# Optimization experiments

Measured on AMD Instinct MI355X. Metric: run time of the kernel, lower is better.

Reference implementation:

```python
import jax, jax.numpy as jnp
import numpy as np

EPS = 1.1920928955078125e-07  # torch fp32 default eps for F.rms_norm
N_HEADS = 16
HEAD_DIM = 128


def apply_rotary_emb(x, cos, sin):
    # x: [B,S,H,D]; cos/sin: [1,S,1,D/2]
    d = x.shape[-1] // 2
    x1, x2 = x[..., :d], x[..., d:]
    return jnp.concatenate([x1 * cos + x2 * sin, -x1 * sin + x2 * cos], axis=-1)


def rms_norm(x):
    # F.rms_norm over last dim, no learned weight
    ms = jnp.mean(jnp.square(x), axis=-1, keepdims=True)
    return x * jax.lax.rsqrt(ms + EPS)


def setup_inputs() -> dict:
    key = jax.random.key(0)
    ks = jax.random.split(key, 7)
    B, S, D = 2, 2048, 2048
    half = HEAD_DIM // 2
    # rotary tables (built like standard RoPE for realism)
    inv_freq = 1.0 / (10000.0 ** (np.arange(0, half, dtype=np.float32) / half))
    t = np.arange(S, dtype=np.float32)
    freqs = np.outer(t, inv_freq)  # [S, D/2]
    cos = jnp.asarray(np.cos(freqs))[None, :, None, :]
    sin = jnp.asarray(np.sin(freqs))[None, :, None, :]
    sd = 1.0 / np.sqrt(D)
    return {
        "x": jax.random.normal(ks[0], (B, S, D), jnp.float32),
        "cos": cos,
        "sin": sin,
        "Wq": jax.random.normal(ks[1], (D, D), jnp.float32) * sd,
        "Wk": jax.random.normal(ks[2], (D, D), jnp.float32) * sd,
        "Wv": jax.random.normal(ks[3], (D, D), jnp.float32) * sd,
        "Wo": jax.random.normal(ks[4], (D, D), jnp.float32) * sd,
    }


def reference(x, cos, sin, Wq, Wk, Wv, Wo):
    B, S, D = x.shape
    H, Hd = N_HEADS, HEAD_DIM
    q = (x @ Wq.T).reshape(B, S, H, Hd)
    k = (x @ Wk.T).reshape(B, S, H, Hd)
    v = (x @ Wv.T).reshape(B, S, H, Hd)
    q = apply_rotary_emb(q, cos[:, :S], sin[:, :S])
    k = apply_rotary_emb(k, cos[:, :S], sin[:, :S])
    q = rms_norm(q) * 1.2  # [B,S,H,Hd]
    k = rms_norm(k) * 1.2
    scale = 1.0 / jnp.sqrt(jnp.asarray(Hd, x.dtype))
    # scores: [B,H,Sq,Sk]
    scores = jnp.einsum("bqhd,bkhd->bhqk", q, k) * scale
    attn = jax.nn.softmax(scores, axis=-1)
    y = jnp.einsum("bhqk,bkhd->bqhd", attn, v).reshape(B, S, D)
    return y @ Wo.T
```

## Files before the change

### kernel.cpp

```cpp
#include <hip/hip_runtime.h>
#include <hip/hip_bf16.h>
#include <math.h>

typedef __bf16 bf16;
typedef __attribute__((ext_vector_type(8))) __bf16 bf16x8;
typedef __attribute__((ext_vector_type(4))) float f32x4;
typedef __attribute__((ext_vector_type(16))) float f32x16;

#define DEV __device__ __forceinline__

DEV void gload16(const void* g, void* l) {
    __builtin_amdgcn_global_load_lds(
        (__attribute__((address_space(1))) void*)(void*)g,
        (__attribute__((address_space(3))) void*)l, 16, 0, 0);
}

DEV unsigned pk2(float a, float b) {
    union { bf16 h[2]; unsigned u; } z;
    z.h[0] = (bf16)a; z.h[1] = (bf16)b;
    return z.u;
}

DEV void plswap(unsigned& a, unsigned& b) {
    asm volatile("v_permlane32_swap_b32 %0, %1" : "+v"(a), "+v"(b));
}

DEV f32x16 mfma32(bf16x8 a, bf16x8 b, f32x16 c) {
    return __builtin_amdgcn_mfma_f32_32x32x16_bf16(a, b, c, 0, 0, 0);
}

__global__ __launch_bounds__(256) void cvt_kernel(const float* __restrict__ in,
                                                  bf16* __restrict__ out, int n8) {
    for (int i = blockIdx.x * 256 + threadIdx.x; i < n8; i += gridDim.x * 256) {
        const float4* p = (const float4*)(in + (size_t)i * 8);
        float4 a = p[0], b = p[1];
        bf16x8 o;
        o[0] = (bf16)a.x; o[1] = (bf16)a.y; o[2] = (bf16)a.z; o[3] = (bf16)a.w;
        o[4] = (bf16)b.x; o[5] = (bf16)b.y; o[6] = (bf16)b.z; o[7] = (bf16)b.w;
        *(bf16x8*)(out + (size_t)i * 8) = o;
    }
}

__global__ __launch_bounds__(256) void cvtw_kernel(const float* __restrict__ w0,
                                                   const float* __restrict__ w1,
                                                   const float* __restrict__ w2,
                                                   const float* __restrict__ w3,
                                                   bf16* __restrict__ out) {
    const float* in = (blockIdx.y == 0) ? w0 : (blockIdx.y == 1) ? w1
                      : (blockIdx.y == 2) ? w2 : w3;
    bf16* o = out + (size_t)blockIdx.y * 4194304;
    for (int i = blockIdx.x * 256 + threadIdx.x; i < 524288; i += 512 * 256) {
        const float4* p = (const float4*)(in + (size_t)i * 8);
        float4 a = p[0], b = p[1];
        bf16x8 v;
        v[0] = (bf16)a.x; v[1] = (bf16)a.y; v[2] = (bf16)a.z; v[3] = (bf16)a.w;
        v[4] = (bf16)b.x; v[5] = (bf16)b.y; v[6] = (bf16)b.z; v[7] = (bf16)b.w;
        *(bf16x8*)(o + (size_t)i * 8) = v;
    }
}

__global__ __launch_bounds__(512, 2) void gemm_qkv(const bf16* __restrict__ A,
                                                   const bf16* __restrict__ Bg,
                                                   bf16* __restrict__ outq) {
    __shared__ __align__(16) bf16 As[3][256 * 32];
    __shared__ __align__(16) bf16 Bs[3][384 * 32];
    const int tid = threadIdx.x, lane = tid & 63, wv = tid >> 6;
    const int q31 = lane & 31, h5 = lane >> 5;
    const int wm = wv >> 2, wn = wv & 3;
    const int K = 2048;

    int lin = blockIdx.x;
    int swz = (lin & 7) * 32 + (lin >> 3);
    const int tm = (swz >> 4) * 256;
    const int tn = (swz & 15) * 384;

    f32x16 acc[4][3] = {};

    auto stageA = [&](int t, int buf) {
#pragma unroll
        for (int l = 0; l < 2; ++l) {
            int chunk = l * 8 + wv;
            int row = chunk * 16 + (lane >> 2);
            int cb = ((lane & 3) * 16) ^ (((row >> 1) & 3) << 4);
            gload16((const char*)(A + (size_t)(tm + row) * K + t * 32) + cb,
                    (char*)(As[buf]) + chunk * 1024);
        }
    };
    auto stageB = [&](int t, int buf) {
#pragma unroll
        for (int l = 0; l < 3; ++l) {
            int chunk = l * 8 + wv;
            int row = chunk * 16 + (lane >> 2);
            int cb = ((lane & 3) * 16) ^ (((row >> 1) & 3) << 4);
            gload16((const char*)(Bg + (size_t)(tn + row) * K + t * 32) + cb,
                    (char*)(Bs[buf]) + chunk * 1024);
        }
    };
    auto rdA = [&](int buf, int mb, int ks) -> bf16x8 {
        int row = wm * 128 + mb * 32 + q31;
        int off = (ks * 32 + h5 * 16) ^ (((row >> 1) & 3) << 4);
        return *(const bf16x8*)((const char*)(As[buf]) + row * 64 + off);
    };
    auto rdB = [&](int buf, int nb, int ks) -> bf16x8 {
        int row = wn * 96 + nb * 32 + q31;
        int off = (ks * 32 + h5 * 16) ^ (((row >> 1) & 3) << 4);
        return *(const bf16x8*)((const char*)(Bs[buf]) + row * 64 + off);
    };

    stageA(0, 0); stageB(0, 0);
    stageA(1, 1); stageB(1, 1);
    asm volatile("s_waitcnt vmcnt(5)" ::: "memory");
    __builtin_amdgcn_s_barrier();

    int cur = 0, nxt2 = 2;
    for (int t = 0; t < 64; ++t) {
        bf16x8 af[2][2], bfr[3][2];
#pragma unroll
        for (int mb = 0; mb < 2; ++mb)
#pragma unroll
            for (int ks = 0; ks < 2; ++ks) af[mb][ks] = rdA(cur, mb, ks);
#pragma unroll
        for (int nb = 0; nb < 3; ++nb)
#pragma unroll
            for (int ks = 0; ks < 2; ++ks) bfr[nb][ks] = rdB(cur, nb, ks);
        if (t < 62) stageA(t + 2, nxt2);
        __builtin_amdgcn_s_barrier();
        asm volatile("s_waitcnt lgkmcnt(0)" ::: "memory");
        __builtin_amdgcn_sched_barrier(0);
        __builtin_amdgcn_s_setprio(1);
#pragma unroll
        for (int mb = 0; mb < 2; ++mb)
#pragma unroll
            for (int nb = 0; nb < 3; ++nb)
#pragma unroll
                for (int ks = 0; ks < 2; ++ks)
                    acc[mb][nb] = mfma32(af[mb][ks], bfr[nb][ks], acc[mb][nb]);
        __builtin_amdgcn_s_setprio(0);
        __builtin_amdgcn_s_barrier();
#pragma unroll
        for (int mb = 0; mb < 2; ++mb)
#pragma unroll
            for (int ks = 0; ks < 2; ++ks) af[mb][ks] = rdA(cur, 2 + mb, ks);
        if (t < 62) stageB(t + 2, nxt2);
        __builtin_amdgcn_s_barrier();
        asm volatile("s_waitcnt lgkmcnt(0)" ::: "memory");
        __builtin_amdgcn_sched_barrier(0);
        __builtin_amdgcn_s_setprio(1);
#pragma unroll
        for (int mb = 0; mb < 2; ++mb)
#pragma unroll
            for (int nb = 0; nb < 3; ++nb)
#pragma unroll
                for (int ks = 0; ks < 2; ++ks)
                    acc[2 + mb][nb] = mfma32(af[mb][ks], bfr[nb][ks], acc[2 + mb][nb]);
        __builtin_amdgcn_s_setprio(0);
        if (t < 62)
            asm volatile("s_waitcnt vmcnt(5)" ::: "memory");
        else
            asm volatile("s_waitcnt vmcnt(0)" ::: "memory");
        __builtin_amdgcn_s_barrier();
        cur = (cur == 2) ? 0 : cur + 1;
        nxt2 = (nxt2 == 2) ? 0 : nxt2 + 1;
    }

#pragma unroll
    for (int mb = 0; mb < 4; ++mb)
#pragma unroll
        for (int nb = 0; nb < 3; ++nb) {
            int colbase = tn + wn * 96 + nb * 32;
            bf16* op = outq + (size_t)(colbase >> 11) * 8388608 +
                       (colbase & 2047) + q31;
#pragma unroll
            for (int r = 0; r < 16; ++r) {
                int row = tm + wm * 128 + mb * 32 + (r & 3) + 8 * (r >> 2) + 4 * h5;
                op[(size_t)row * 2048] = (bf16)acc[mb][nb][r];
            }
        }
}

template <bool F32OUT>
__global__ __launch_bounds__(256) void gemm_bt(const bf16* __restrict__ A,
                                               const bf16* __restrict__ B,
                                               void* __restrict__ Cout,
                                               int M, int N, int K) {
    __shared__ __align__(16) bf16 As[128 * 64];
    __shared__ __align__(16) bf16 Bs[128 * 64];
    const int tid = threadIdx.x, lane = tid & 63, wv = tid >> 6;
    const int tm = blockIdx.y * 128, tn = blockIdx.x * 128;
    const int wr = (wv >> 1) * 64, wc = (wv & 1) * 64;

    f32x4 acc[4][4] = {};
    const int scb = (lane & 7) * 16;

    for (int k0 = 0; k0 < K; k0 += 64) {
#pragma unroll
        for (int i = 0; i < 4; ++i) {
            int chunk = wv * 4 + i;
            int row = chunk * 8 + (lane >> 3);
            int cb = scb ^ ((row & 7) << 4);
            gload16((const char*)(A + (size_t)(tm + row) * K + k0) + cb,
                    (char*)As + chunk * 1024);
            gload16((const char*)(B + (size_t)(tn + row) * K + k0) + cb,
                    (char*)Bs + chunk * 1024);
        }
        __syncthreads();
#pragma unroll
        for (int kk = 0; kk < 2; ++kk) {
            bf16x8 af[4], bfr[4];
#pragma unroll
            for (int m = 0; m < 4; ++m) {
                int row = wr + m * 16 + (lane & 15);
                int cb = (kk * 64 + ((lane >> 4) * 16)) ^ ((row & 7) << 4);
                af[m] = *(const bf16x8*)((const char*)As + row * 128 + cb);
            }
#pragma unroll
            for (int n = 0; n < 4; ++n) {
                int row = wc + n * 16 + (lane & 15);
                int cb = (kk * 64 + ((lane >> 4) * 16)) ^ ((row & 7) << 4);
                bfr[n] = *(const bf16x8*)((const char*)Bs + row * 128 + cb);
            }
#pragma unroll
            for (int m = 0; m < 4; ++m)
#pragma unroll
                for (int n = 0; n < 4; ++n)
                    acc[m][n] = __builtin_amdgcn_mfma_f32_16x16x32_bf16(
                        af[m], bfr[n], acc[m][n], 0, 0, 0);
        }
        __syncthreads();
    }
#pragma unroll
    for (int m = 0; m < 4; ++m)
#pragma unroll
        for (int n = 0; n < 4; ++n)
#pragma unroll
            for (int r = 0; r < 4; ++r) {
                int row = tm + wr + m * 16 + (lane >> 4) * 4 + r;
                int col = tn + wc + n * 16 + (lane & 15);
                if (F32OUT)
                    ((float*)Cout)[(size_t)row * N + col] = acc[m][n][r];
                else
                    ((bf16*)Cout)[(size_t)row * N + col] = (bf16)acc[m][n][r];
            }
}

__global__ __launch_bounds__(256) void rope_rms(bf16* __restrict__ q,
                                                bf16* __restrict__ k,
                                                const float* __restrict__ cosp,
                                                const float* __restrict__ sinp) {
    int gw = blockIdx.x * 4 + (threadIdx.x >> 6);
    int lane = threadIdx.x & 63;
    bf16* base = (blockIdx.y == 0) ? q : k;
    int m = gw >> 4, h = gw & 15;
    int s = m & 2047;
    bf16* p = base + (size_t)m * 2048 + h * 128;
    float x1 = (float)p[lane], x2 = (float)p[lane + 64];
    float c = cosp[s * 64 + lane], si = sinp[s * 64 + lane];
    float r1 = x1 * c + x2 * si;
    float r2 = x2 * c - x1 * si;
    float ss = r1 * r1 + r2 * r2;
#pragma unroll
    for (int msk = 1; msk < 64; msk <<= 1) ss += __shfl_xor(ss, msk);
    float sc = rsqrtf(ss * (1.0f / 128.0f) + 1.1920928955078125e-07f) * 1.2f;
    if (blockIdx.y == 0) sc *= (0.08838834764831845f * 1.4426950408889634f);
    p[lane] = (bf16)(r1 * sc);
    p[lane + 64] = (bf16)(r2 * sc);
}

__global__ __launch_bounds__(256, 2) void attn_kernel(const bf16* __restrict__ q,
                                                      const bf16* __restrict__ k,
                                                      const bf16* __restrict__ v,
                                                      bf16* __restrict__ y) {
    __shared__ __align__(16) bf16 Ks[2][64 * 128];
    __shared__ __align__(16) bf16 Vt[2][128][72];

    const int tid = threadIdx.x, lane = tid & 63, wv = tid >> 6;
    const int q31 = lane & 31, h5 = lane >> 5;

    int wgid = blockIdx.y * 16 + blockIdx.x;
    int xcd = wgid & 7, j = wgid >> 3;
    int bh = xcd * 4 + (j >> 4);
    int qblk = j & 15;
    const int b = bh >> 4, h = bh & 15;
    const int q0 = qblk * 128;

    const bf16* qptr = q + (size_t)(b * 2048 + q0 + wv * 32 + q31) * 2048 +
                       h * 128 + h5 * 8;
    bf16x8 qf[8];
#pragma unroll
    for (int ks = 0; ks < 8; ++ks) qf[ks] = *(const bf16x8*)(qptr + ks * 16);

    float mrun = -INFINITY, lrun = 0.f;
    f32x16 acco[4] = {};

    const bf16* vbase = v + (size_t)(b * 2048 + wv * 16) * 2048 + h * 128 + 2 * lane;
    const bf16* kbase = k + (size_t)(b * 2048) * 2048 + h * 128;

    unsigned u[16];

    auto stageK = [&](int t, int buf) {
#pragma unroll
        for (int i = 0; i < 4; ++i) {
            int chunk = wv * 4 + i;
            int row = chunk * 4 + (lane >> 4);
            int cb = ((lane & 15) * 16) ^ ((row & 7) << 4);
            gload16((const char*)(kbase + (size_t)(t * 64 + row) * 2048) + cb,
                    (char*)(Ks[buf]) + chunk * 1024);
        }
    };
    auto loadV = [&](int t) {
        const bf16* vp = vbase + (size_t)(t * 64) * 2048;
#pragma unroll
        for (int jj = 0; jj < 16; ++jj)
            u[jj] = *(const unsigned*)(vp + (size_t)jj * 2048);
    };
    auto writeV = [&](int buf) {
        union { unsigned short s[8]; bf16x8 v8; } r0a, r0b, r1a, r1b;
#pragma unroll
        for (int jj = 0; jj < 8; ++jj) {
            r0a.s[jj] = (unsigned short)(u[jj] & 0xffff);
            r1a.s[jj] = (unsigned short)(u[jj] >> 16);
            r0b.s[jj] = (unsigned short)(u[jj + 8] & 0xffff);
            r1b.s[jj] = (unsigned short)(u[jj + 8] >> 16);
        }
        *(bf16x8*)(&Vt[buf][2 * lane][wv * 16]) = r0a.v8;
        *(bf16x8*)(&Vt[buf][2 * lane][wv * 16 + 8]) = r0b.v8;
        *(bf16x8*)(&Vt[buf][2 * lane + 1][wv * 16]) = r1a.v8;
        *(bf16x8*)(&Vt[buf][2 * lane + 1][wv * 16 + 8]) = r1b.v8;
    };

    stageK(0, 0);
    loadV(0);
    writeV(0);
    __syncthreads();

    for (int t = 0; t < 32; ++t) {
        const int c = t & 1;
        if (t < 31) {
            stageK(t + 1, c ^ 1);
            loadV(t + 1);
        }

        f32x16 st[2];
        __builtin_amdgcn_s_setprio(1);
#pragma unroll
        for (int kvb = 0; kvb < 2; ++kvb) {
            f32x16 a = {};
#pragma unroll
            for (int ks = 0; ks < 8; ++ks) {
                int row = kvb * 32 + q31;
                int cb = (32 * ks + 16 * h5) ^ ((row & 7) << 4);
                const bf16x8 kf =
                    *(const bf16x8*)((const char*)(Ks[c]) + row * 256 + cb);
                a = __builtin_amdgcn_mfma_f32_32x32x16_bf16(kf, qf[ks], a, 0, 0, 0);
            }
            st[kvb] = a;
        }
        __builtin_amdgcn_s_setprio(0);

        float t8[8];
#pragma unroll
        for (int r = 0; r < 8; ++r)
            t8[r] = fmaxf(fmaxf(st[0][r], st[0][r + 8]),
                          fmaxf(st[1][r], st[1][r + 8]));
        float mx = fmaxf(fmaxf(fmaxf(t8[0], t8[1]), fmaxf(t8[2], t8[3])),
                         fmaxf(fmaxf(t8[4], t8[5]), fmaxf(t8[6], t8[7])));
        mx = fmaxf(mx, __shfl_xor(mx, 32));

        if (__any(mx - mrun > 8.0f)) {
            float mn = fmaxf(mrun, mx);
            float alpha = exp2f(mrun - mn);
            mrun = mn;
            lrun *= alpha;
#pragma unroll
            for (int r = 0; r < 16; ++r) {
                int qr = (r & 3) + 8 * (r >> 2) + 4 * h5;
                float al = __shfl(alpha, qr);
                acco[0][r] *= al; acco[1][r] *= al;
                acco[2][r] *= al; acco[3][r] *= al;
            }
        }

        unsigned w[2][8];
        float rsa = 0.f, rsb = 0.f;
#pragma unroll
        for (int kvb = 0; kvb < 2; ++kvb)
#pragma unroll
            for (int i = 0; i < 8; ++i) {
                float p0 = exp2f(st[kvb][2 * i] - mrun);
                float p1 = exp2f(st[kvb][2 * i + 1] - mrun);
                if (i & 1) rsb += p0 + p1; else rsa += p0 + p1;
                w[kvb][i] = pk2(p0, p1);
            }
        float rs = rsa + rsb;
        rs += __shfl_xor(rs, 32);
        lrun += rs;

        __builtin_amdgcn_s_setprio(1);
#pragma unroll
        for (int b2 = 0; b2 < 2; ++b2)
#pragma unroll
            for (int ksl = 0; ksl < 2; ++ksl) {
                const int ks = b2 * 2 + ksl, u0 = ksl * 4;
                unsigned f0 = w[b2][u0 + 0], f2 = w[b2][u0 + 2];
                unsigned f1 = w[b2][u0 + 1], f3 = w[b2][u0 + 3];
                plswap(f0, f2);
                plswap(f1, f3);
                union { unsigned uu[4]; bf16x8 v8; } fr;
                fr.uu[0] = f0; fr.uu[1] = f1; fr.uu[2] = f2; fr.uu[3] = f3;
#pragma unroll
                for (int dblk = 0; dblk < 4; ++dblk) {
                    const bf16x8 vf = *(const bf16x8*)(
                        &Vt[c][dblk * 32 + q31][ks * 16 + h5 * 8]);
                    acco[dblk] = __builtin_amdgcn_mfma_f32_32x32x16_bf16(
                        fr.v8, vf, acco[dblk], 0, 0, 0);
                }
            }
        __builtin_amdgcn_s_setprio(0);

        if (t < 31) writeV(c ^ 1);
        __syncthreads();
    }

    float linv = 1.0f / lrun;
#pragma unroll
    for (int r = 0; r < 16; ++r) {
        int qr = (r & 3) + 8 * (r >> 2) + 4 * h5;
        float il = __shfl(linv, qr);
        size_t row = (size_t)(b * 2048 + q0 + wv * 32 + qr) * 2048 + h * 128;
#pragma unroll
        for (int dblk = 0; dblk < 4; ++dblk)
            y[row + dblk * 32 + q31] = (bf16)(acco[dblk][r] * il);
    }
}

extern "C" void kernel_launch(void* const* d_in, const int* in_sizes, int n_in,
                              void* d_out, int out_size, void* d_ws, size_t ws_size,
                              hipStream_t stream) {
    const float* x = (const float*)d_in[0];
    const float* cs = (const float*)d_in[1];
    const float* sn = (const float*)d_in[2];
    const float* Wq = (const float*)d_in[3];
    const float* Wk = (const float*)d_in[4];
    const float* Wv = (const float*)d_in[5];
    const float* Wo = (const float*)d_in[6];

    char* ws = (char*)d_ws;
    bf16* xb  = (bf16*)(ws + 0);
    bf16* wqb = (bf16*)(ws + 16777216);
    bf16* wob = (bf16*)(ws + 41943040);
    bf16* qb  = (bf16*)(ws + 50331648);
    bf16* kb  = (bf16*)(ws + 67108864);
    bf16* vb  = (bf16*)(ws + 83886080);
    bf16* yb  = (bf16*)(ws + 100663296);

    cvt_kernel<<<1024, 256, 0, stream>>>(x, xb, 8388608 / 8);
    cvtw_kernel<<<dim3(512, 4), 256, 0, stream>>>(Wq, Wk, Wv, Wo, wqb);

    gemm_qkv<<<256, 512, 0, stream>>>(xb, wqb, qb);

    rope_rms<<<dim3(16384, 2), 256, 0, stream>>>(qb, kb, cs, sn);

    attn_kernel<<<dim3(16, 32), 256, 0, stream>>>(qb, kb, vb, yb);

    dim3 g(16, 32);
    gemm_bt<true><<<g, 256, 0, stream>>>(yb, wob, d_out, 4096, 2048, 2048);
}
```

Before: 288.8 us.

## Widen attention blocks to 256 queries and swizzle V LDS and GEMM tiles

The attention kernel now uses 512 threads (8 waves) per block covering 256 query rows, so each staged K/V tile is shared by twice as many queries and global K/V traffic is halved. V transpose staging is split across 8 row groups, and an XOR swizzle is applied to the Vt LDS writes and reads to reduce bank conflicts. The output-projection GEMM also remaps block IDs so consecutive blocks on each XCD share row tiles, aiming for better L2 reuse. The larger blocks raise register pressure under the tighter launch bounds and halve the block count to 256.

Result: slower. 496.4 us (+71.9%).

```diff
diff --git a/kernel.cpp b/kernel.cpp
--- a/kernel.cpp
+++ b/kernel.cpp
@@ -186,7 +186,9 @@
     __shared__ __align__(16) bf16 As[128 * 64];
     __shared__ __align__(16) bf16 Bs[128 * 64];
     const int tid = threadIdx.x, lane = tid & 63, wv = tid >> 6;
-    const int tm = blockIdx.y * 128, tn = blockIdx.x * 128;
+    int lin = blockIdx.y * 16 + blockIdx.x;
+    int swz = (lin & 7) * 64 + (lin >> 3);
+    const int tm = (swz >> 4) * 128, tn = (swz & 15) * 128;
     const int wr = (wv >> 1) * 64, wc = (wv & 1) * 64;
 
     f32x4 acc[4][4] = {};
@@ -266,7 +268,7 @@
     p[lane + 64] = (bf16)(r2 * sc);
 }
 
-__global__ __launch_bounds__(256, 2) void attn_kernel(const bf16* __restrict__ q,
+__global__ __launch_bounds__(512, 4) void attn_kernel(const bf16* __restrict__ q,
                                                       const bf16* __restrict__ k,
                                                       const bf16* __restrict__ v,
                                                       bf16* __restrict__ y) {
@@ -276,12 +278,12 @@
     const int tid = threadIdx.x, lane = tid & 63, wv = tid >> 6;
     const int q31 = lane & 31, h5 = lane >> 5;
 
-    int wgid = blockIdx.y * 16 + blockIdx.x;
+    int wgid = blockIdx.y * 8 + blockIdx.x;
     int xcd = wgid & 7, j = wgid >> 3;
-    int bh = xcd * 4 + (j >> 4);
-    int qblk = j & 15;
+    const int bh = xcd * 4 + (j >> 3);
+    const int qblk = j & 7;
     const int b = bh >> 4, h = bh & 15;
-    const int q0 = qblk * 128;
+    const int q0 = qblk * 256;
 
     const bf16* qptr = q + (size_t)(b * 2048 + q0 + wv * 32 + q31) * 2048 +
                        h * 128 + h5 * 8;
@@ -292,15 +294,17 @@
     float mrun = -INFINITY, lrun = 0.f;
     f32x16 acco[4] = {};
 
-    const bf16* vbase = v + (size_t)(b * 2048 + wv * 16) * 2048 + h * 128 + 2 * lane;
+    const int p = tid & 63, rg = tid >> 6;
+    const bf16* vbase = v + (size_t)(b * 2048 + rg * 8) * 2048 + h * 128 + 2 * p;
     const bf16* kbase = k + (size_t)(b * 2048) * 2048 + h * 128;
-
-    unsigned u[16];
+    const int vx = ((p >> 2) & 1) << 5;
+
+    unsigned u[8];
 
     auto stageK = [&](int t, int buf) {
 #pragma unroll
-        for (int i = 0; i < 4; ++i) {
-            int chunk = wv * 4 + i;
+        for (int i = 0; i < 2; ++i) {
+            int chunk = wv * 2 + i;
             int row = chunk * 4 + (lane >> 4);
             int cb = ((lane & 15) * 16) ^ ((row & 7) << 4);
             gload16((const char*)(kbase + (size_t)(t * 64 + row) * 2048) + cb,
@@ -310,28 +314,28 @@
     auto loadV = [&](int t) {
         const bf16* vp = vbase + (size_t)(t * 64) * 2048;
 #pragma unroll
-        for (int jj = 0; jj < 16; ++jj)
+        for (int jj = 0; jj < 8; ++jj)
             u[jj] = *(const unsigned*)(vp + (size_t)jj * 2048);
     };
     auto writeV = [&](int buf) {
-        union { unsigned short s[8]; bf16x8 v8; } r0a, r0b, r1a, r1b;
+        union { unsigned short s[8]; bf16x8 v8; } lo, hi;
 #pragma unroll
         for (int jj = 0; jj < 8; ++jj) {
-            r0a.s[jj] = (unsigned short)(u[jj] & 0xffff);
-            r1a.s[jj] = (unsigned short)(u[jj] >> 16);
-            r0b.s[jj] = (unsigned short)(u[jj + 8] & 0xffff);
-            r1b.s[jj] = (unsigned short)(u[jj + 8] >> 16);
-        }
-        *(bf16x8*)(&Vt[buf][2 * lane][wv * 16]) = r0a.v8;
-        *(bf16x8*)(&Vt[buf][2 * lane][wv * 16 + 8]) = r0b.v8;
-        *(bf16x8*)(&Vt[buf][2 * lane + 1][wv * 16]) = r1a.v8;
-        *(bf16x8*)(&Vt[buf][2 * lane + 1][wv * 16 + 8]) = r1b.v8;
+            lo.s[jj] = (unsigned short)(u[jj] & 0xffff);
+            hi.s[jj] = (unsigned short)(u[jj] >> 16);
+        }
+        char* r0 = (char*)(&Vt[buf][2 * p][0]);
+        char* r1 = (char*)(&Vt[buf][2 * p + 1][0]);
+        *(bf16x8*)(r0 + ((rg * 16) ^ vx)) = lo.v8;
+        *(bf16x8*)(r1 + ((rg * 16) ^ vx)) = hi.v8;
     };
 
     stageK(0, 0);
     loadV(0);
     writeV(0);
     __syncthreads();
+
+    const int rx = ((q31 >> 3) & 1) << 5;
 
     for (int t = 0; t < 32; ++t) {
         const int c = t & 1;
@@ -409,8 +413,9 @@
                 fr.uu[0] = f0; fr.uu[1] = f1; fr.uu[2] = f2; fr.uu[3] = f3;
 #pragma unroll
                 for (int dblk = 0; dblk < 4; ++dblk) {
-                    const bf16x8 vf = *(const bf16x8*)(
-                        &Vt[c][dblk * 32 + q31][ks * 16 + h5 * 8]);
+                    const char* vrow = (const char*)(&Vt[c][dblk * 32 + q31][0]);
+                    const bf16x8 vf =
+                        *(const bf16x8*)(vrow + ((ks * 32 + h5 * 16) ^ rx));
                     acco[dblk] = __builtin_amdgcn_mfma_f32_32x32x16_bf16(
                         fr.v8, vf, acco[dblk], 0, 0, 0);
                 }
@@ -460,7 +465,7 @@
 
     rope_rms<<<dim3(16384, 2), 256, 0, stream>>>(qb, kb, cs, sn);
 
-    attn_kernel<<<dim3(16, 32), 256, 0, stream>>>(qb, kb, vb, yb);
+    attn_kernel<<<dim3(8, 32), 512, 0, stream>>>(qb, kb, vb, yb);
 
     dim3 g(16, 32);
     gemm_bt<true><<<g, 256, 0, stream>>>(yb, wob, d_out, 4096, 2048, 2048);
```
